# Performance work log

Hardware: AMD Instinct MI355X
Metric: run time of the kernel (lower is better)

The kernel has to match this reference:

```python
import jax, jax.numpy as jnp
import numpy as np

N = 50000      # num nodes
E = 800000     # num edges (avg degree 16)
D = 128        # feature dim
HOP = 2        # number of propagation hops
FILL = 0.5     # self-loop fill value (A_hat = A + fill*I)


def setup_inputs() -> dict:
    key = jax.random.key(0)
    k1, k2, k3, k4, k5 = jax.random.split(key, 5)
    x_s = jax.random.normal(k1, (N, D), dtype=jnp.float32)
    x_t = jax.random.normal(k2, (N, D), dtype=jnp.float32)
    src = jax.random.randint(k3, (E,), 0, N)
    # guarantee no pre-existing self-loops so that appending all self-loops
    # exactly matches add_remaining_self_loops
    dst = (src + jax.random.randint(k4, (E,), 1, N)) % N
    edge_index = jnp.stack([src, dst]).astype(jnp.int32)
    edge_weight = jax.random.uniform(k5, (E,), dtype=jnp.float32)
    # DIMPA parameters, initialized to 1.0 per _reset_parameters
    w_s = jnp.ones((HOP + 1, 1), dtype=jnp.float32)
    w_t = jnp.ones((HOP + 1, 1), dtype=jnp.float32)
    return {"x_s": x_s, "x_t": x_t, "edge_index": edge_index,
            "edge_weight": edge_weight, "w_s": w_s, "w_t": w_t}


def _conv(x, row, col, w, n, fill):
    # Conv_Base: add self loops with weight `fill`, row-normalize by weighted
    # out-degree of `row`, scatter-add messages w_norm * x[row] onto `col`.
    loop = jnp.arange(n, dtype=row.dtype)
    row_a = jnp.concatenate([row, loop])
    col_a = jnp.concatenate([col, loop])
    w_a = jnp.concatenate([w, jnp.full((n,), fill, dtype=w.dtype)])
    deg = jax.ops.segment_sum(w_a, row_a, num_segments=n)
    deg_inv = jnp.where(deg == 0, jnp.zeros_like(deg), 1.0 / deg)  # inf -> 0
    w_norm = deg_inv[row_a] * w_a                                   # [E+n]
    return jax.ops.segment_sum(w_norm[:, None] * x[row_a], col_a, num_segments=n)


def reference(x_s, x_t, edge_index, edge_weight, w_s, w_t):
    n = x_s.shape[0]
    row, col = edge_index[0], edge_index[1]
    feat_s = w_s[0] * x_s
    feat_t = w_t[0] * x_t
    curr_s, curr_t = x_s, x_t
    for h in range(1, HOP + 1):
        curr_s = _conv(curr_s, row, col, edge_weight, n, FILL)
        # edge_index_t = edge_index[[1, 0]] -> swap row/col
        curr_t = _conv(curr_t, col, row, edge_weight, n, FILL)
        feat_s = feat_s + w_s[h] * curr_s
        feat_t = feat_t + w_t[h] * curr_t
    return jnp.concatenate([feat_s, feat_t], axis=1)  # [N, 2D]
```

## Files before the change

kernel.cpp:

```cpp
#include <hip/hip_runtime.h>

#define D 128
#define FILLV 0.5f
#define NXCD 8
#define EPT 8

#define CNT_SHIFT 22
#define DEG_MASK  0x3FFFFFu

typedef unsigned short u16;
typedef unsigned long long u64;
typedef unsigned uv4 __attribute__((ext_vector_type(4)));
typedef u64 u64v2 __attribute__((ext_vector_type(2)));

__device__ __forceinline__ u16 f2bf(float f) {
    unsigned u = __float_as_uint(f);
    u += 0x7FFF + ((u >> 16) & 1);
    return (u16)(u >> 16);
}
__device__ __forceinline__ float bf2f(u16 h) {
    return __uint_as_float(((unsigned)h) << 16);
}

__global__ void cnt_tobf_kernel(const int* __restrict__ row, const int* __restrict__ col,
                                const float* __restrict__ w,
                                unsigned* __restrict__ cnt32, unsigned* __restrict__ ranks,
                                const float* __restrict__ x_s, const float* __restrict__ x_t,
                                u16* __restrict__ xb_s, u16* __restrict__ xb_t,
                                int E, int N, int nEB, long long nd) {
    if ((int)blockIdx.x < nEB) {
        long long g  = (long long)blockIdx.x * 256 + threadIdx.x;
        long long e0 = g * EPT;
        if (e0 >= E) return;
        if (e0 + EPT <= E && (E & 3) == 0) {
            int rr[EPT]; int cc[EPT]; unsigned fx[EPT];
            #pragma unroll
            for (int h = 0; h < EPT / 4; ++h) {
                int q = (int)(e0 >> 2) + h;
                int4   r4 = *(const int4*)(row + 4 * (size_t)q);
                int4   c4 = *(const int4*)(col + 4 * (size_t)q);
                float4 w4 = *(const float4*)(w + 4 * (size_t)q);
                rr[4*h] = r4.x; rr[4*h+1] = r4.y; rr[4*h+2] = r4.z; rr[4*h+3] = r4.w;
                cc[4*h] = c4.x; cc[4*h+1] = c4.y; cc[4*h+2] = c4.z; cc[4*h+3] = c4.w;
                fx[4*h]   = (unsigned)(w4.x * 65536.0f);
                fx[4*h+1] = (unsigned)(w4.y * 65536.0f);
                fx[4*h+2] = (unsigned)(w4.z * 65536.0f);
                fx[4*h+3] = (unsigned)(w4.w * 65536.0f);
            }
            unsigned oc[EPT], orr[EPT];
            #pragma unroll
            for (int k = 0; k < EPT; ++k) {
                unsigned add = (1u << CNT_SHIFT) | fx[k];
                oc[k]  = atomicAdd(&cnt32[(size_t)cc[k]], add);
                orr[k] = atomicAdd(&cnt32[(size_t)N + rr[k]], add);
            }
            unsigned pk[EPT];
            #pragma unroll
            for (int k = 0; k < EPT; ++k)
                pk[k] = ((orr[k] >> CNT_SHIFT) << 16) | (oc[k] >> CNT_SHIFT);
            uv4 pa = {pk[0], pk[1], pk[2], pk[3]};
            uv4 pb = {pk[4], pk[5], pk[6], pk[7]};
            __builtin_nontemporal_store(pa, (uv4*)(ranks + e0));
            __builtin_nontemporal_store(pb, (uv4*)(ranks + e0 + 4));
        } else {
            for (long long e = e0; e < E && e < e0 + EPT; ++e) {
                int r = row[e], c = col[e];
                unsigned add = (1u << CNT_SHIFT) | (unsigned)(w[e] * 65536.0f);
                unsigned oc  = atomicAdd(&cnt32[(size_t)c], add);
                unsigned orr = atomicAdd(&cnt32[(size_t)N + r], add);
                ranks[e] = ((orr >> CNT_SHIFT) << 16) | (oc >> CNT_SHIFT);
            }
        }
    } else {
        long long t = (long long)(blockIdx.x - nEB) * 256 + threadIdx.x;
        long long q = nd / 4;
        const float* x; u16* xb; long long i;
        if (t < q) { x = x_s; xb = xb_s; i = t * 4; }
        else if (t < 2 * q) { x = x_t; xb = xb_t; i = (t - q) * 4; }
        else return;
        float4 v = *(const float4*)(x + i);
        ushort4 o;
        o.x = f2bf(v.x); o.y = f2bf(v.y); o.z = f2bf(v.z); o.w = f2bf(v.w);
        *(ushort4*)(xb + i) = o;
    }
}

__global__ void scanAI_kernel(unsigned* __restrict__ cnt32, float* __restrict__ dinv,
                              int* __restrict__ tsum, int total) {
    __shared__ int sh[256];
    int gid = blockIdx.x * 256 + threadIdx.x;
    int cnt = 0;
    if (gid < total) {
        unsigned v = cnt32[gid];
        float deg = (float)(v & DEG_MASK) * (1.0f / 65536.0f);
        dinv[gid] = 1.0f / (deg + FILLV);
        cnt = (int)(v >> CNT_SHIFT);
        cnt32[gid] = (unsigned)cnt;
    }
    sh[threadIdx.x] = cnt;
    __syncthreads();
    for (int off = 128; off > 0; off >>= 1) {
        if (threadIdx.x < off) sh[threadIdx.x] += sh[threadIdx.x + off];
        __syncthreads();
    }
    if (threadIdx.x == 0) tsum[blockIdx.x] = sh[0];
}

__global__ void scanC_kernel(const unsigned* __restrict__ cnt32, const int* __restrict__ tsum,
                             int* __restrict__ start, int total, int grand_total) {
    __shared__ int sh[256];
    int acc = 0;
    for (int j = threadIdx.x; j < (int)blockIdx.x; j += 256) acc += tsum[j];
    sh[threadIdx.x] = acc;
    __syncthreads();
    for (int off = 128; off > 0; off >>= 1) {
        if (threadIdx.x < off) sh[threadIdx.x] += sh[threadIdx.x + off];
        __syncthreads();
    }
    int bpref = sh[0];
    __syncthreads();
    int gid = blockIdx.x * 256 + threadIdx.x;
    int v = (gid < total) ? (int)cnt32[gid] : 0;
    sh[threadIdx.x] = v;
    __syncthreads();
    for (int off = 1; off < 256; off <<= 1) {
        int u = 0;
        if (threadIdx.x >= off) u = sh[threadIdx.x - off];
        __syncthreads();
        sh[threadIdx.x] += u;
        __syncthreads();
    }
    int run = bpref + sh[threadIdx.x] - v;
    if (gid < total) start[gid] = run;
    if (gid == 0) start[total] = grand_total;
}

__global__ void slot2_kernel(const int* __restrict__ start,
                             const int* __restrict__ row, const int* __restrict__ col,
                             const float* __restrict__ w, const unsigned* __restrict__ ranks,
                             const float* __restrict__ dinv,
                             unsigned* __restrict__ cursor,
                             unsigned* __restrict__ bslot, u64* __restrict__ bpay,
                             int E, int N, int SL) {
    __shared__ unsigned hist[NXCD];
    __shared__ unsigned wbase[NXCD];
    if (threadIdx.x < NXCD) hist[threadIdx.x] = 0;
    __syncthreads();
    long long g  = (long long)blockIdx.x * 256 + threadIdx.x;
    long long e0 = g * 4;
    unsigned rslot[8]; u64 rpay[8]; unsigned rbin[8], rrank[8];
    int nrec = 0;
    if (e0 < E) {
        if (e0 + 4 <= E && (E & 3) == 0) {
            int q = (int)(e0 >> 2);
            int4   r4 = *(const int4*)(row + 4 * (size_t)q);
            int4   c4 = *(const int4*)(col + 4 * (size_t)q);
            float4 w4 = *(const float4*)(w + 4 * (size_t)q);
            uv4    p4 = __builtin_nontemporal_load((const uv4*)(ranks + e0));
            int rr[4] = {r4.x, r4.y, r4.z, r4.w};
            int cc[4] = {c4.x, c4.y, c4.z, c4.w};
            float ww[4] = {w4.x, w4.y, w4.z, w4.w};
            unsigned pk[4] = {p4.x, p4.y, p4.z, p4.w};
            #pragma unroll
            for (int k = 0; k < 4; ++k) {
                int ss = start[cc[k]] + (int)(pk[k] & 0xffffu);
                int st = start[N + rr[k]] + (int)(pk[k] >> 16);
                float wns = ww[k] * dinv[N + rr[k]];
                float wnt = ww[k] * dinv[cc[k]];
                rslot[nrec] = (unsigned)ss;
                rpay[nrec]  = ((u64)__float_as_uint(wns) << 32) | (unsigned)rr[k];
                ++nrec;
                rslot[nrec] = (unsigned)st;
                rpay[nrec]  = ((u64)__float_as_uint(wnt) << 32) | (unsigned)cc[k];
                ++nrec;
            }
        } else {
            for (long long e = e0; e < E && e < e0 + 4; ++e) {
                int r = row[e], c = col[e];
                float we = w[e];
                unsigned pk = ranks[e];
                int ss = start[c] + (int)(pk & 0xffffu);
                int st = start[N + r] + (int)(pk >> 16);
                float wns = we * dinv[N + r];
                float wnt = we * dinv[c];
                rslot[nrec] = (unsigned)ss;
                rpay[nrec]  = ((u64)__float_as_uint(wns) << 32) | (unsigned)r;
                ++nrec;
                rslot[nrec] = (unsigned)st;
                rpay[nrec]  = ((u64)__float_as_uint(wnt) << 32) | (unsigned)c;
                ++nrec;
            }
        }
        for (int j = 0; j < nrec; ++j) {
            rbin[j]  = rslot[j] / (unsigned)SL;
            rrank[j] = atomicAdd(&hist[rbin[j]], 1u);
        }
    }
    __syncthreads();
    if (threadIdx.x < NXCD)
        wbase[threadIdx.x] = atomicAdd(&cursor[threadIdx.x], hist[threadIdx.x]);
    __syncthreads();
    for (int j = 0; j < nrec; ++j) {
        unsigned pos = rbin[j] * (unsigned)SL + wbase[rbin[j]] + rrank[j];
        bslot[pos] = rslot[j];
        bpay[pos]  = rpay[j];
    }
}

__global__ void fill2_kernel(const unsigned* __restrict__ bslot, const u64* __restrict__ bpay,
                             u64* __restrict__ edges, int E2, int SL) {
    int rid = blockIdx.x & 7;
    long long idx = ((long long)(blockIdx.x >> 3) * 256 + threadIdx.x) * 2;
    long long lo  = (long long)rid * SL;
    long long rem = (long long)E2 - lo;
    int cntb = rem < 0 ? 0 : (rem > SL ? SL : (int)rem);
    if (idx >= cntb) return;
    long long p = lo + idx;
    if (idx + 2 <= cntb) {
        u64   s2 = __builtin_nontemporal_load((const u64*)(bslot + p));
        u64v2 y2 = __builtin_nontemporal_load((const u64v2*)(bpay + p));
        unsigned s0 = (unsigned)(s2 & 0xffffffffu), s1 = (unsigned)(s2 >> 32);
        edges[s0] = y2[0];
        edges[s1] = y2[1];
    } else {
        edges[bslot[p]] = __builtin_nontemporal_load(bpay + p);
    }
}

__global__ void pull1_kernel(const int* __restrict__ start, const int2* __restrict__ edges,
                             const float* __restrict__ dinv,
                             const u16* __restrict__ xb_s, const u16* __restrict__ xb_t,
                             const float* __restrict__ x_s, const float* __restrict__ x_t,
                             u16* __restrict__ ab_s, u16* __restrict__ ab_t, int N) {
    int wid0 = (int)(((long long)blockIdx.x * blockDim.x + threadIdx.x) >> 6);
    int wid = __builtin_amdgcn_readfirstlane(wid0);
    int lane = threadIdx.x & 63;
    int half = lane >> 5, hl = lane & 31;
    if (wid >= 2 * N) return;
    const u16* xb; const float* x; u16* ab; int i, o;
    if (wid < N) { i = wid;     o = N; xb = xb_s; x = x_s; ab = ab_s; }
    else         { i = wid - N; o = 0; xb = xb_t; x = x_t; ab = ab_t; }
    int s0 = start[wid], s1 = start[wid + 1];
    float a0 = 0.f, a1 = 0.f, a2 = 0.f, a3 = 0.f;
    int k = s0;
    for (; k + 8 <= s1; k += 8) {
        int b = k + 4 * half;
        int2 p0 = edges[b], p1 = edges[b + 1], p2 = edges[b + 2], p3 = edges[b + 3];
        ushort4 v0 = *(const ushort4*)(xb + (size_t)p0.x * D + hl * 4);
        ushort4 v1 = *(const ushort4*)(xb + (size_t)p1.x * D + hl * 4);
        ushort4 v2 = *(const ushort4*)(xb + (size_t)p2.x * D + hl * 4);
        ushort4 v3 = *(const ushort4*)(xb + (size_t)p3.x * D + hl * 4);
        float w0v = __int_as_float(p0.y), w1v = __int_as_float(p1.y);
        float w2v = __int_as_float(p2.y), w3v = __int_as_float(p3.y);
        a0 += w0v * bf2f(v0.x) + w1v * bf2f(v1.x) + w2v * bf2f(v2.x) + w3v * bf2f(v3.x);
        a1 += w0v * bf2f(v0.y) + w1v * bf2f(v1.y) + w2v * bf2f(v2.y) + w3v * bf2f(v3.y);
        a2 += w0v * bf2f(v0.z) + w1v * bf2f(v1.z) + w2v * bf2f(v2.z) + w3v * bf2f(v3.z);
        a3 += w0v * bf2f(v0.w) + w1v * bf2f(v1.w) + w2v * bf2f(v2.w) + w3v * bf2f(v3.w);
    }
    if (k + 4 <= s1) {
        int b = k + 2 * half;
        int2 p0 = edges[b], p1 = edges[b + 1];
        ushort4 v0 = *(const ushort4*)(xb + (size_t)p0.x * D + hl * 4);
        ushort4 v1 = *(const ushort4*)(xb + (size_t)p1.x * D + hl * 4);
        float w0v = __int_as_float(p0.y), w1v = __int_as_float(p1.y);
        a0 += w0v * bf2f(v0.x) + w1v * bf2f(v1.x);
        a1 += w0v * bf2f(v0.y) + w1v * bf2f(v1.y);
        a2 += w0v * bf2f(v0.z) + w1v * bf2f(v1.z);
        a3 += w0v * bf2f(v0.w) + w1v * bf2f(v1.w);
        k += 4;
    }
    for (; k < s1; ++k) {
        if (half == 0) {
            int2 p = edges[k];
            ushort4 v = *(const ushort4*)(xb + (size_t)p.x * D + hl * 4);
            float wv = __int_as_float(p.y);
            a0 += wv * bf2f(v.x); a1 += wv * bf2f(v.y);
            a2 += wv * bf2f(v.z); a3 += wv * bf2f(v.w);
        }
    }
    a0 += __shfl_xor(a0, 32); a1 += __shfl_xor(a1, 32);
    a2 += __shfl_xor(a2, 32); a3 += __shfl_xor(a3, 32);
    if (half == 0) {
        float sw = FILLV * dinv[o + i];
        float4 xv = *(const float4*)(x + (size_t)i * D + hl * 4);
        a0 += sw * xv.x; a1 += sw * xv.y; a2 += sw * xv.z; a3 += sw * xv.w;
        ushort4 ov;
        ov.x = f2bf(a0); ov.y = f2bf(a1); ov.z = f2bf(a2); ov.w = f2bf(a3);
        *(ushort4*)(ab + (size_t)i * D + hl * 4) = ov;
    }
}

__global__ void pull2_kernel(const int* __restrict__ start, const int2* __restrict__ edges,
                             const float* __restrict__ dinv,
                             const u16* __restrict__ ab_s, const u16* __restrict__ ab_t,
                             const float* __restrict__ x_s, const float* __restrict__ x_t,
                             float* __restrict__ out,
                             const float* __restrict__ w_s, const float* __restrict__ w_t, int N) {
    int wid0 = (int)(((long long)blockIdx.x * blockDim.x + threadIdx.x) >> 6);
    int wid = __builtin_amdgcn_readfirstlane(wid0);
    int lane = threadIdx.x & 63;
    int half = lane >> 5, hl = lane & 31;
    if (wid >= 2 * N) return;
    const u16* ab; const float* x; const float* wv3; int i, o, hoff;
    if (wid < N) { i = wid;     o = N; ab = ab_s; x = x_s; wv3 = w_s; hoff = 0; }
    else         { i = wid - N; o = 0; ab = ab_t; x = x_t; wv3 = w_t; hoff = D; }
    int s0 = start[wid], s1 = start[wid + 1];
    float a0 = 0.f, a1 = 0.f, a2 = 0.f, a3 = 0.f;
    int k = s0;
    for (; k + 8 <= s1; k += 8) {
        int b = k + 4 * half;
        int2 p0 = edges[b], p1 = edges[b + 1], p2 = edges[b + 2], p3 = edges[b + 3];
        ushort4 v0 = *(const ushort4*)(ab + (size_t)p0.x * D + hl * 4);
        ushort4 v1 = *(const ushort4*)(ab + (size_t)p1.x * D + hl * 4);
        ushort4 v2 = *(const ushort4*)(ab + (size_t)p2.x * D + hl * 4);
        ushort4 v3 = *(const ushort4*)(ab + (size_t)p3.x * D + hl * 4);
        float w0v = __int_as_float(p0.y), w1v = __int_as_float(p1.y);
        float w2v = __int_as_float(p2.y), w3v = __int_as_float(p3.y);
        a0 += w0v * bf2f(v0.x) + w1v * bf2f(v1.x) + w2v * bf2f(v2.x) + w3v * bf2f(v3.x);
        a1 += w0v * bf2f(v0.y) + w1v * bf2f(v1.y) + w2v * bf2f(v2.y) + w3v * bf2f(v3.y);
        a2 += w0v * bf2f(v0.z) + w1v * bf2f(v1.z) + w2v * bf2f(v2.z) + w3v * bf2f(v3.z);
        a3 += w0v * bf2f(v0.w) + w1v * bf2f(v1.w) + w2v * bf2f(v2.w) + w3v * bf2f(v3.w);
    }
    if (k + 4 <= s1) {
        int b = k + 2 * half;
        int2 p0 = edges[b], p1 = edges[b + 1];
        ushort4 v0 = *(const ushort4*)(ab + (size_t)p0.x * D + hl * 4);
        ushort4 v1 = *(const ushort4*)(ab + (size_t)p1.x * D + hl * 4);
        float w0v = __int_as_float(p0.y), w1v = __int_as_float(p1.y);
        a0 += w0v * bf2f(v0.x) + w1v * bf2f(v1.x);
        a1 += w0v * bf2f(v0.y) + w1v * bf2f(v1.y);
        a2 += w0v * bf2f(v0.z) + w1v * bf2f(v1.z);
        a3 += w0v * bf2f(v0.w) + w1v * bf2f(v1.w);
        k += 4;
    }
    for (; k < s1; ++k) {
        if (half == 0) {
            int2 p = edges[k];
            ushort4 v = *(const ushort4*)(ab + (size_t)p.x * D + hl * 4);
            float wv = __int_as_float(p.y);
            a0 += wv * bf2f(v.x); a1 += wv * bf2f(v.y);
            a2 += wv * bf2f(v.z); a3 += wv * bf2f(v.w);
        }
    }
    a0 += __shfl_xor(a0, 32); a1 += __shfl_xor(a1, 32);
    a2 += __shfl_xor(a2, 32); a3 += __shfl_xor(a3, 32);
    if (half == 0) {
        float sw = FILLV * dinv[o + i];
        ushort4 av = *(const ushort4*)(ab + (size_t)i * D + hl * 4);
        float b0 = bf2f(av.x), b1 = bf2f(av.y), b2 = bf2f(av.z), b3 = bf2f(av.w);
        a0 += sw * b0; a1 += sw * b1; a2 += sw * b2; a3 += sw * b3;
        float w0 = wv3[0], w1 = wv3[1], w2 = wv3[2];
        float4 xv = *(const float4*)(x + (size_t)i * D + hl * 4);
        float4 ov;
        ov.x = w0 * xv.x + w1 * b0 + w2 * a0;
        ov.y = w0 * xv.y + w1 * b1 + w2 * a1;
        ov.z = w0 * xv.z + w1 * b2 + w2 * a2;
        ov.w = w0 * xv.w + w1 * b3 + w2 * a3;
        *(float4*)(out + (size_t)i * 2 * D + hoff + hl * 4) = ov;
    }
}

extern "C" void kernel_launch(void* const* d_in, const int* in_sizes, int n_in,
                              void* d_out, int out_size, void* d_ws, size_t ws_size,
                              hipStream_t stream) {
    const float* x_s = (const float*)d_in[0];
    const float* x_t = (const float*)d_in[1];
    const int*   ei  = (const int*)d_in[2];
    const float* ew  = (const float*)d_in[3];
    const float* w_s = (const float*)d_in[4];
    const float* w_t = (const float*)d_in[5];
    const int N = in_sizes[0] / D;
    const int E = in_sizes[3];
    const int* row = ei;
    const int* col = ei + E;

    const int total = 2 * N;
    const int nTiles = (total + 255) / 256;
    const int SL = ((2 * E + NXCD - 1) / NXCD + 7) & ~7;

    float* f      = (float*)d_ws;
    float* dinv   = f;
    int*   start  = (int*)(f + (size_t)total);
    int*   tsum   = start + (total + 2);
    char*  pc     = (char*)(tsum + 512);
    pc = (char*)(((size_t)pc + 255) & ~(size_t)255);
    u64*   edges  = (u64*)pc;
    u16*   xb_s   = (u16*)(edges + 2 * (size_t)E);
    u16*   xb_t   = xb_s + (size_t)N * D;
    u16*   ab_s   = xb_t + (size_t)N * D;
    u16*   ab_t   = ab_s + (size_t)N * D;
    unsigned* cnt32  = (unsigned*)ab_s;
    unsigned* cursor = cnt32 + (size_t)total;

    unsigned* ranks = (unsigned*)d_out;
    char* po = (char*)d_out + (((size_t)E * 4 + 15) & ~(size_t)15);
    unsigned* bslot = (unsigned*)po;
    u64*      bpay  = (u64*)(bslot + (size_t)NXCD * SL);
    float* out = (float*)d_out;

    hipMemsetAsync(cnt32, 0, ((size_t)total + NXCD) * sizeof(unsigned), stream);

    long long nd = (long long)N * D;
    int blkC = (int)((nd / 2 + 255) / 256);
    int nEB  = (E + EPT * 256 - 1) / (EPT * 256);
    cnt_tobf_kernel<<<nEB + blkC, 256, 0, stream>>>(row, col, ew, cnt32, ranks,
                                                    x_s, x_t, xb_s, xb_t,
                                                    E, N, nEB, nd);
    scanAI_kernel<<<nTiles, 256, 0, stream>>>(cnt32, dinv, tsum, total);
    scanC_kernel<<<nTiles, 256, 0, stream>>>(cnt32, tsum, start, total, 2 * E);

    int blkS = (E + 1023) / 1024;
    slot2_kernel<<<blkS, 256, 0, stream>>>(start, row, col, ew, ranks, dinv,
                                           cursor, bslot, bpay, E, N, SL);

    int blkF = 8 * ((SL + 511) / 512);
    fill2_kernel<<<blkF, 256, 0, stream>>>(bslot, bpay, edges, 2 * E, SL);

    long long pull_threads = (long long)total * 64;
    int blkP = (int)((pull_threads + 255) / 256);
    pull1_kernel<<<blkP, 256, 0, stream>>>(start, (const int2*)edges, dinv, xb_s, xb_t,
                                           x_s, x_t, ab_s, ab_t, N);
    pull2_kernel<<<blkP, 256, 0, stream>>>(start, (const int2*)edges, dinv, ab_s, ab_t,
                                           x_s, x_t, out, w_s, w_t, N);
}
```

Measured before the change: 337.4 us.

## Fuse scan, slot and fill stages into one cooperative kernel with grid syncs

Replaces four separate launches (the two scan passes, the slot bucketing and the fill scatter) with one cooperative kernel. Grid-wide barriers separate the phases, and the scan and fill phases use grid-stride loops so that a fixed grid sized to the edge count covers all the work. The aim is to remove inter-kernel launch gaps and drain/refill time. In exchange it pays for three grid.sync barriers, and it requires every block to be co-resident; the launch return code is not checked, so a failed cooperative launch would go unnoticed.

```diff
diff --git a/kernel.cpp b/kernel.cpp
--- a/kernel.cpp
+++ b/kernel.cpp
@@ -1,4 +1,7 @@
 #include <hip/hip_runtime.h>
+#include <hip/hip_cooperative_groups.h>
+
+namespace cg = cooperative_groups;
 
 #define D 128
 #define FILLV 0.5f
@@ -85,145 +88,157 @@
     }
 }
 
-__global__ void scanAI_kernel(unsigned* __restrict__ cnt32, float* __restrict__ dinv,
-                              int* __restrict__ tsum, int total) {
+__global__ void mid_kernel(unsigned* __restrict__ cnt32, float* __restrict__ dinv,
+                           int* __restrict__ tsum, int* __restrict__ start,
+                           const int* __restrict__ row, const int* __restrict__ col,
+                           const float* __restrict__ w, const unsigned* __restrict__ ranks,
+                           unsigned* __restrict__ cursor,
+                           unsigned* __restrict__ bslot, u64* __restrict__ bpay,
+                           u64* __restrict__ edges,
+                           int E, int N, int SL, int nTiles, int total, int grand_total) {
     __shared__ int sh[256];
-    int gid = blockIdx.x * 256 + threadIdx.x;
-    int cnt = 0;
-    if (gid < total) {
-        unsigned v = cnt32[gid];
-        float deg = (float)(v & DEG_MASK) * (1.0f / 65536.0f);
-        dinv[gid] = 1.0f / (deg + FILLV);
-        cnt = (int)(v >> CNT_SHIFT);
-        cnt32[gid] = (unsigned)cnt;
-    }
-    sh[threadIdx.x] = cnt;
-    __syncthreads();
-    for (int off = 128; off > 0; off >>= 1) {
-        if (threadIdx.x < off) sh[threadIdx.x] += sh[threadIdx.x + off];
-        __syncthreads();
-    }
-    if (threadIdx.x == 0) tsum[blockIdx.x] = sh[0];
-}
-
-__global__ void scanC_kernel(const unsigned* __restrict__ cnt32, const int* __restrict__ tsum,
-                             int* __restrict__ start, int total, int grand_total) {
-    __shared__ int sh[256];
-    int acc = 0;
-    for (int j = threadIdx.x; j < (int)blockIdx.x; j += 256) acc += tsum[j];
-    sh[threadIdx.x] = acc;
-    __syncthreads();
-    for (int off = 128; off > 0; off >>= 1) {
-        if (threadIdx.x < off) sh[threadIdx.x] += sh[threadIdx.x + off];
-        __syncthreads();
-    }
-    int bpref = sh[0];
-    __syncthreads();
-    int gid = blockIdx.x * 256 + threadIdx.x;
-    int v = (gid < total) ? (int)cnt32[gid] : 0;
-    sh[threadIdx.x] = v;
-    __syncthreads();
-    for (int off = 1; off < 256; off <<= 1) {
-        int u = 0;
-        if (threadIdx.x >= off) u = sh[threadIdx.x - off];
-        __syncthreads();
-        sh[threadIdx.x] += u;
-        __syncthreads();
-    }
-    int run = bpref + sh[threadIdx.x] - v;
-    if (gid < total) start[gid] = run;
-    if (gid == 0) start[total] = grand_total;
-}
-
-__global__ void slot2_kernel(const int* __restrict__ start,
-                             const int* __restrict__ row, const int* __restrict__ col,
-                             const float* __restrict__ w, const unsigned* __restrict__ ranks,
-                             const float* __restrict__ dinv,
-                             unsigned* __restrict__ cursor,
-                             unsigned* __restrict__ bslot, u64* __restrict__ bpay,
-                             int E, int N, int SL) {
     __shared__ unsigned hist[NXCD];
     __shared__ unsigned wbase[NXCD];
-    if (threadIdx.x < NXCD) hist[threadIdx.x] = 0;
-    __syncthreads();
-    long long g  = (long long)blockIdx.x * 256 + threadIdx.x;
-    long long e0 = g * 4;
-    unsigned rslot[8]; u64 rpay[8]; unsigned rbin[8], rrank[8];
-    int nrec = 0;
-    if (e0 < E) {
-        if (e0 + 4 <= E && (E & 3) == 0) {
-            int q = (int)(e0 >> 2);
-            int4   r4 = *(const int4*)(row + 4 * (size_t)q);
-            int4   c4 = *(const int4*)(col + 4 * (size_t)q);
-            float4 w4 = *(const float4*)(w + 4 * (size_t)q);
-            uv4    p4 = __builtin_nontemporal_load((const uv4*)(ranks + e0));
-            int rr[4] = {r4.x, r4.y, r4.z, r4.w};
-            int cc[4] = {c4.x, c4.y, c4.z, c4.w};
-            float ww[4] = {w4.x, w4.y, w4.z, w4.w};
-            unsigned pk[4] = {p4.x, p4.y, p4.z, p4.w};
-            #pragma unroll
-            for (int k = 0; k < 4; ++k) {
-                int ss = start[cc[k]] + (int)(pk[k] & 0xffffu);
-                int st = start[N + rr[k]] + (int)(pk[k] >> 16);
-                float wns = ww[k] * dinv[N + rr[k]];
-                float wnt = ww[k] * dinv[cc[k]];
-                rslot[nrec] = (unsigned)ss;
-                rpay[nrec]  = ((u64)__float_as_uint(wns) << 32) | (unsigned)rr[k];
-                ++nrec;
-                rslot[nrec] = (unsigned)st;
-                rpay[nrec]  = ((u64)__float_as_uint(wnt) << 32) | (unsigned)cc[k];
-                ++nrec;
-            }
-        } else {
-            for (long long e = e0; e < E && e < e0 + 4; ++e) {
-                int r = row[e], c = col[e];
-                float we = w[e];
-                unsigned pk = ranks[e];
-                int ss = start[c] + (int)(pk & 0xffffu);
-                int st = start[N + r] + (int)(pk >> 16);
-                float wns = we * dinv[N + r];
-                float wnt = we * dinv[c];
-                rslot[nrec] = (unsigned)ss;
-                rpay[nrec]  = ((u64)__float_as_uint(wns) << 32) | (unsigned)r;
-                ++nrec;
-                rslot[nrec] = (unsigned)st;
-                rpay[nrec]  = ((u64)__float_as_uint(wnt) << 32) | (unsigned)c;
-                ++nrec;
-            }
-        }
+    cg::grid_group grid = cg::this_grid();
+    const int tid = threadIdx.x;
+
+    for (int tile = blockIdx.x; tile < nTiles; tile += gridDim.x) {
+        int gid = tile * 256 + tid;
+        int cnt = 0;
+        if (gid < total) {
+            unsigned v = cnt32[gid];
+            float deg = (float)(v & DEG_MASK) * (1.0f / 65536.0f);
+            dinv[gid] = 1.0f / (deg + FILLV);
+            cnt = (int)(v >> CNT_SHIFT);
+            cnt32[gid] = (unsigned)cnt;
+        }
+        sh[tid] = cnt;
+        __syncthreads();
+        for (int off = 128; off > 0; off >>= 1) {
+            if (tid < off) sh[tid] += sh[tid + off];
+            __syncthreads();
+        }
+        if (tid == 0) tsum[tile] = sh[0];
+        __syncthreads();
+    }
+    grid.sync();
+
+    for (int tile = blockIdx.x; tile < nTiles; tile += gridDim.x) {
+        int acc = 0;
+        for (int j = tid; j < tile; j += 256) acc += tsum[j];
+        sh[tid] = acc;
+        __syncthreads();
+        for (int off = 128; off > 0; off >>= 1) {
+            if (tid < off) sh[tid] += sh[tid + off];
+            __syncthreads();
+        }
+        int bpref = sh[0];
+        __syncthreads();
+        int gid = tile * 256 + tid;
+        int v = (gid < total) ? (int)cnt32[gid] : 0;
+        sh[tid] = v;
+        __syncthreads();
+        for (int off = 1; off < 256; off <<= 1) {
+            int u = 0;
+            if (tid >= off) u = sh[tid - off];
+            __syncthreads();
+            sh[tid] += u;
+            __syncthreads();
+        }
+        int run = bpref + sh[tid] - v;
+        if (gid < total) start[gid] = run;
+        if (gid == 0) start[total] = grand_total;
+        __syncthreads();
+    }
+    grid.sync();
+
+    {
+        if (tid < NXCD) hist[tid] = 0;
+        __syncthreads();
+        long long g  = (long long)blockIdx.x * 256 + tid;
+        long long e0 = g * 4;
+        unsigned rslot[8]; u64 rpay[8]; unsigned rbin[8], rrank[8];
+        int nrec = 0;
+        if (e0 < E) {
+            if (e0 + 4 <= E && (E & 3) == 0) {
+                int q = (int)(e0 >> 2);
+                int4   r4 = *(const int4*)(row + 4 * (size_t)q);
+                int4   c4 = *(const int4*)(col + 4 * (size_t)q);
+                float4 w4 = *(const float4*)(w + 4 * (size_t)q);
+                uv4    p4 = __builtin_nontemporal_load((const uv4*)(ranks + e0));
+                int rr[4] = {r4.x, r4.y, r4.z, r4.w};
+                int cc[4] = {c4.x, c4.y, c4.z, c4.w};
+                float ww[4] = {w4.x, w4.y, w4.z, w4.w};
+                unsigned pk[4] = {p4.x, p4.y, p4.z, p4.w};
+                #pragma unroll
+                for (int k = 0; k < 4; ++k) {
+                    int ss = start[cc[k]] + (int)(pk[k] & 0xffffu);
+                    int st = start[N + rr[k]] + (int)(pk[k] >> 16);
+                    float wns = ww[k] * dinv[N + rr[k]];
+                    float wnt = ww[k] * dinv[cc[k]];
+                    rslot[nrec] = (unsigned)ss;
+                    rpay[nrec]  = ((u64)__float_as_uint(wns) << 32) | (unsigned)rr[k];
+                    ++nrec;
+                    rslot[nrec] = (unsigned)st;
+                    rpay[nrec]  = ((u64)__float_as_uint(wnt) << 32) | (unsigned)cc[k];
+                    ++nrec;
+                }
+            } else {
+                for (long long e = e0; e < E && e < e0 + 4; ++e) {
+                    int r = row[e], c = col[e];
+                    float we = w[e];
+                    unsigned pk = ranks[e];
+                    int ss = start[c] + (int)(pk & 0xffffu);
+                    int st = start[N + r] + (int)(pk >> 16);
+                    float wns = we * dinv[N + r];
+                    float wnt = we * dinv[c];
+                    rslot[nrec] = (unsigned)ss;
+                    rpay[nrec]  = ((u64)__float_as_uint(wns) << 32) | (unsigned)r;
+                    ++nrec;
+                    rslot[nrec] = (unsigned)st;
+                    rpay[nrec]  = ((u64)__float_as_uint(wnt) << 32) | (unsigned)c;
+                    ++nrec;
+                }
+            }
+            for (int j = 0; j < nrec; ++j) {
+                rbin[j]  = rslot[j] / (unsigned)SL;
+                rrank[j] = atomicAdd(&hist[rbin[j]], 1u);
+            }
+        }
+        __syncthreads();
+        if (tid < NXCD)
+            wbase[tid] = atomicAdd(&cursor[tid], hist[tid]);
+        __syncthreads();
         for (int j = 0; j < nrec; ++j) {
-            rbin[j]  = rslot[j] / (unsigned)SL;
-            rrank[j] = atomicAdd(&hist[rbin[j]], 1u);
-        }
-    }
-    __syncthreads();
-    if (threadIdx.x < NXCD)
-        wbase[threadIdx.x] = atomicAdd(&cursor[threadIdx.x], hist[threadIdx.x]);
-    __syncthreads();
-    for (int j = 0; j < nrec; ++j) {
-        unsigned pos = rbin[j] * (unsigned)SL + wbase[rbin[j]] + rrank[j];
-        bslot[pos] = rslot[j];
-        bpay[pos]  = rpay[j];
-    }
-}
-
-__global__ void fill2_kernel(const unsigned* __restrict__ bslot, const u64* __restrict__ bpay,
-                             u64* __restrict__ edges, int E2, int SL) {
-    int rid = blockIdx.x & 7;
-    long long idx = ((long long)(blockIdx.x >> 3) * 256 + threadIdx.x) * 2;
-    long long lo  = (long long)rid * SL;
-    long long rem = (long long)E2 - lo;
-    int cntb = rem < 0 ? 0 : (rem > SL ? SL : (int)rem);
-    if (idx >= cntb) return;
-    long long p = lo + idx;
-    if (idx + 2 <= cntb) {
-        u64   s2 = __builtin_nontemporal_load((const u64*)(bslot + p));
-        u64v2 y2 = __builtin_nontemporal_load((const u64v2*)(bpay + p));
-        unsigned s0 = (unsigned)(s2 & 0xffffffffu), s1 = (unsigned)(s2 >> 32);
-        edges[s0] = y2[0];
-        edges[s1] = y2[1];
-    } else {
-        edges[bslot[p]] = __builtin_nontemporal_load(bpay + p);
+            unsigned pos = rbin[j] * (unsigned)SL + wbase[rbin[j]] + rrank[j];
+            bslot[pos] = rslot[j];
+            bpay[pos]  = rpay[j];
+        }
+    }
+    grid.sync();
+
+    {
+        int g8 = (int)(gridDim.x >> 3);
+        if ((int)blockIdx.x < (g8 << 3)) {
+            int rid = blockIdx.x & 7;
+            int nchunk = (SL + 511) / 512;
+            long long lo  = (long long)rid * SL;
+            long long rem = (long long)(2 * E) - lo;
+            int cntb = rem < 0 ? 0 : (rem > SL ? SL : (int)rem);
+            for (int chunk = blockIdx.x >> 3; chunk < nchunk; chunk += g8) {
+                long long idx = ((long long)chunk * 256 + tid) * 2;
+                if (idx >= cntb) continue;
+                long long p = lo + idx;
+                if (idx + 2 <= cntb) {
+                    u64   s2 = __builtin_nontemporal_load((const u64*)(bslot + p));
+                    u64v2 y2 = __builtin_nontemporal_load((const u64v2*)(bpay + p));
+                    edges[(unsigned)(s2 & 0xffffffffu)] = y2[0];
+                    edges[(unsigned)(s2 >> 32)] = y2[1];
+                } else {
+                    edges[bslot[p]] = __builtin_nontemporal_load(bpay + p);
+                }
+            }
+        }
     }
 }
 
@@ -406,15 +421,16 @@
     cnt_tobf_kernel<<<nEB + blkC, 256, 0, stream>>>(row, col, ew, cnt32, ranks,
                                                     x_s, x_t, xb_s, xb_t,
                                                     E, N, nEB, nd);
-    scanAI_kernel<<<nTiles, 256, 0, stream>>>(cnt32, dinv, tsum, total);
-    scanC_kernel<<<nTiles, 256, 0, stream>>>(cnt32, tsum, start, total, 2 * E);
-
-    int blkS = (E + 1023) / 1024;
-    slot2_kernel<<<blkS, 256, 0, stream>>>(start, row, col, ew, ranks, dinv,
-                                           cursor, bslot, bpay, E, N, SL);
-
-    int blkF = 8 * ((SL + 511) / 512);
-    fill2_kernel<<<blkF, 256, 0, stream>>>(bslot, bpay, edges, 2 * E, SL);
+
+    const int blkMid = (E + 1023) / 1024;
+    const int grand_total = 2 * E;
+    void* margs[] = {(void*)&cnt32, (void*)&dinv, (void*)&tsum, (void*)&start,
+                     (void*)&row, (void*)&col, (void*)&ew, (void*)&ranks,
+                     (void*)&cursor, (void*)&bslot, (void*)&bpay, (void*)&edges,
+                     (void*)&E, (void*)&N, (void*)&SL, (void*)&nTiles,
+                     (void*)&total, (void*)&grand_total};
+    hipLaunchCooperativeKernel((void*)mid_kernel, dim3(blkMid), dim3(256),
+                               margs, 0, stream);
 
     long long pull_threads = (long long)total * 64;
     int blkP = (int)((pull_threads + 255) / 256);
```

Result: slower. 590.0 us (+74.8%).

## Fuse two-pass scan into single-pass decoupled look-back scan

Applied to the files above, without the earlier changes.

Replaces the reduce-then-scan pair of kernels with one kernel that publishes per-tile aggregates and inclusive prefixes in a flag-tagged state array, which later tiles read with a wavefront look-back. This removes one kernel launch and the second kernel's serial per-block sum over all earlier tile totals. It relies on tiles being scheduled roughly in order for forward progress and on the state array being zeroed by an enlarged memset.

```diff
diff --git a/kernel.cpp b/kernel.cpp
--- a/kernel.cpp
+++ b/kernel.cpp
@@ -85,52 +85,73 @@
     }
 }
 
-__global__ void scanAI_kernel(unsigned* __restrict__ cnt32, float* __restrict__ dinv,
-                              int* __restrict__ tsum, int total) {
+__global__ void scanF_kernel(const unsigned* __restrict__ cnt32, float* __restrict__ dinv,
+                             u64* __restrict__ tstate, int* __restrict__ start,
+                             int total, int grand_total) {
     __shared__ int sh[256];
-    int gid = blockIdx.x * 256 + threadIdx.x;
+    __shared__ int s_prefix;
+    const int tile = blockIdx.x;
+    const int tid  = threadIdx.x;
+    int gid = tile * 256 + tid;
     int cnt = 0;
     if (gid < total) {
         unsigned v = cnt32[gid];
         float deg = (float)(v & DEG_MASK) * (1.0f / 65536.0f);
         dinv[gid] = 1.0f / (deg + FILLV);
         cnt = (int)(v >> CNT_SHIFT);
-        cnt32[gid] = (unsigned)cnt;
-    }
-    sh[threadIdx.x] = cnt;
-    __syncthreads();
-    for (int off = 128; off > 0; off >>= 1) {
-        if (threadIdx.x < off) sh[threadIdx.x] += sh[threadIdx.x + off];
-        __syncthreads();
-    }
-    if (threadIdx.x == 0) tsum[blockIdx.x] = sh[0];
-}
-
-__global__ void scanC_kernel(const unsigned* __restrict__ cnt32, const int* __restrict__ tsum,
-                             int* __restrict__ start, int total, int grand_total) {
-    __shared__ int sh[256];
-    int acc = 0;
-    for (int j = threadIdx.x; j < (int)blockIdx.x; j += 256) acc += tsum[j];
-    sh[threadIdx.x] = acc;
-    __syncthreads();
-    for (int off = 128; off > 0; off >>= 1) {
-        if (threadIdx.x < off) sh[threadIdx.x] += sh[threadIdx.x + off];
-        __syncthreads();
-    }
-    int bpref = sh[0];
-    __syncthreads();
-    int gid = blockIdx.x * 256 + threadIdx.x;
-    int v = (gid < total) ? (int)cnt32[gid] : 0;
-    sh[threadIdx.x] = v;
+    }
+    int orig = cnt;
+    sh[tid] = cnt;
     __syncthreads();
     for (int off = 1; off < 256; off <<= 1) {
         int u = 0;
-        if (threadIdx.x >= off) u = sh[threadIdx.x - off];
+        if (tid >= off) u = sh[tid - off];
         __syncthreads();
-        sh[threadIdx.x] += u;
+        sh[tid] += u;
         __syncthreads();
     }
-    int run = bpref + sh[threadIdx.x] - v;
+    int incl = sh[tid];
+    int local_total = sh[255];
+    if (tid == 0) {
+        u64 pub = ((u64)(unsigned)local_total << 32) | (tile == 0 ? 2u : 1u);
+        __hip_atomic_store(&tstate[tile], pub, __ATOMIC_RELEASE, __HIP_MEMORY_SCOPE_AGENT);
+        if (tile == 0) s_prefix = 0;
+    }
+    if (tile > 0 && tid < 64) {
+        int prefix = 0;
+        int j = tile - 1;
+        for (;;) {
+            int idx = j - tid;
+            u64 st = 0;
+            if (idx >= 0)
+                st = __hip_atomic_load(&tstate[idx], __ATOMIC_ACQUIRE, __HIP_MEMORY_SCOPE_AGENT);
+            unsigned flag = (unsigned)(st & 3u);
+            u64 ball_valid = __ballot(idx < 0 || flag >= 1u);
+            if (ball_valid != ~0ull) continue;
+            u64 ball_incl = __ballot(idx >= 0 && flag == 2u);
+            int val = (idx >= 0) ? (int)(unsigned)(st >> 32) : 0;
+            if (ball_incl) {
+                int c = __ffsll((long long)ball_incl) - 1;
+                int contrib = (tid <= c) ? val : 0;
+                for (int o = 1; o < 64; o <<= 1) contrib += __shfl_xor(contrib, o);
+                prefix += contrib;
+                break;
+            } else {
+                int contrib = val;
+                for (int o = 1; o < 64; o <<= 1) contrib += __shfl_xor(contrib, o);
+                prefix += contrib;
+                j -= 64;
+                if (j < 0) break;
+            }
+        }
+        if (tid == 0) {
+            s_prefix = prefix;
+            u64 pub = ((u64)(unsigned)(prefix + local_total) << 32) | 2u;
+            __hip_atomic_store(&tstate[tile], pub, __ATOMIC_RELEASE, __HIP_MEMORY_SCOPE_AGENT);
+        }
+    }
+    __syncthreads();
+    int run = s_prefix + incl - orig;
     if (gid < total) start[gid] = run;
     if (gid == 0) start[total] = grand_total;
 }
@@ -381,8 +402,7 @@
     float* f      = (float*)d_ws;
     float* dinv   = f;
     int*   start  = (int*)(f + (size_t)total);
-    int*   tsum   = start + (total + 2);
-    char*  pc     = (char*)(tsum + 512);
+    char*  pc     = (char*)(start + total + 2);
     pc = (char*)(((size_t)pc + 255) & ~(size_t)255);
     u64*   edges  = (u64*)pc;
     u16*   xb_s   = (u16*)(edges + 2 * (size_t)E);
@@ -391,6 +411,7 @@
     u16*   ab_t   = ab_s + (size_t)N * D;
     unsigned* cnt32  = (unsigned*)ab_s;
     unsigned* cursor = cnt32 + (size_t)total;
+    u64*      tstate = (u64*)(cursor + NXCD);
 
     unsigned* ranks = (unsigned*)d_out;
     char* po = (char*)d_out + (((size_t)E * 4 + 15) & ~(size_t)15);
@@ -398,7 +419,9 @@
     u64*      bpay  = (u64*)(bslot + (size_t)NXCD * SL);
     float* out = (float*)d_out;
 
-    hipMemsetAsync(cnt32, 0, ((size_t)total + NXCD) * sizeof(unsigned), stream);
+    hipMemsetAsync(cnt32, 0,
+                   ((size_t)total + NXCD) * sizeof(unsigned) + 512 * sizeof(u64),
+                   stream);
 
     long long nd = (long long)N * D;
     int blkC = (int)((nd / 2 + 255) / 256);
@@ -406,8 +429,9 @@
     cnt_tobf_kernel<<<nEB + blkC, 256, 0, stream>>>(row, col, ew, cnt32, ranks,
                                                     x_s, x_t, xb_s, xb_t,
                                                     E, N, nEB, nd);
-    scanAI_kernel<<<nTiles, 256, 0, stream>>>(cnt32, dinv, tsum, total);
-    scanC_kernel<<<nTiles, 256, 0, stream>>>(cnt32, tsum, start, total, 2 * E);
+
+    scanF_kernel<<<nTiles, 256, 0, stream>>>(cnt32, dinv, tstate, start,
+                                             total, 2 * E);
 
     int blkS = (E + 1023) / 1024;
     slot2_kernel<<<blkS, 256, 0, stream>>>(start, row, col, ew, ranks, dinv,
```

Result: slower. 354.7 us (+5.1%).
